# Kernel optimization log

Measured on AMD Instinct MI355X. Metric: run time of the kernel, lower is better.

Reference implementation:

```python
import jax, jax.numpy as jnp
import numpy as np
from jax import lax

B, C_IN, IMG, P = 8, 320, 64, 2
H = W = IMG // P            # 32
N = H * W                   # 1024 tokens
DIM = 128 * P * P           # 512
DEPTH, HEADS, DH = 6, 8, 64
INNER = HEADS * DH          # 512
MLP = 512
EPS = 1e-5


def layernorm(x, g, b):
    mu = x.mean(-1, keepdims=True)
    var = ((x - mu) ** 2).mean(-1, keepdims=True)
    return (x - mu) * lax.rsqrt(var + EPS) * g + b


def conv3x3(x, w, b):
    y = lax.conv_general_dilated(x, w, (1, 1), 'SAME',
                                 dimension_numbers=('NCHW', 'OIHW', 'NCHW'))
    return y + b[None, :, None, None]


def posemb_sincos_2d(h, w, dim, temperature=10000.0):
    y, x = jnp.meshgrid(jnp.arange(h, dtype=jnp.float32),
                        jnp.arange(w, dtype=jnp.float32), indexing='ij')
    omega = jnp.arange(dim // 4, dtype=jnp.float32) / (dim // 4 - 1)
    omega = 1.0 / (temperature ** omega)
    y = y.reshape(-1)[:, None] * omega[None, :]
    x = x.reshape(-1)[:, None] * omega[None, :]
    return jnp.concatenate([jnp.sin(x), jnp.cos(x), jnp.sin(y), jnp.cos(y)], axis=1)


def prepare_attn_mask(mask):
    # attn mask allows position pairs where either row or col token is marked.
    f = 64 // H
    m = (mask == 1)
    r = m.reshape(-1, H, f, W, f).any(axis=(2, 4)).reshape(-1, N)  # [M, N] bool
    return r[:, :, None] | r[:, None, :]                            # [M, N, N]


def setup_inputs() -> dict:
    key = jax.random.key(0)
    ks = jax.random.split(key, 24)
    s = 0.02
    d = dict(
        img=jax.random.normal(ks[0], (B, C_IN, IMG, IMG), jnp.float32),
        mask=jax.random.randint(ks[1], (DEPTH * B, 64, 64), 0, 2, jnp.int32),
        conv1_w=jax.random.normal(ks[2], (128, C_IN, 3, 3), jnp.float32) * s,
        conv1_b=jnp.zeros((128,), jnp.float32),
        ln_p_g=jnp.ones((DIM,), jnp.float32), ln_p_b=jnp.zeros((DIM,), jnp.float32),
        proj_w=jax.random.normal(ks[3], (DIM, DIM), jnp.float32) * s,
        proj_b=jnp.zeros((DIM,), jnp.float32),
        ln_q_g=jnp.ones((DIM,), jnp.float32), ln_q_b=jnp.zeros((DIM,), jnp.float32),
        attn_ln_g=jnp.ones((DEPTH, DIM), jnp.float32),
        attn_ln_b=jnp.zeros((DEPTH, DIM), jnp.float32),
        wqkv=jax.random.normal(ks[4], (DEPTH, DIM, 3 * INNER), jnp.float32) * s,
        wo=jax.random.normal(ks[5], (DEPTH, INNER, DIM), jnp.float32) * s,
        ff_ln_g=jnp.ones((DEPTH, DIM), jnp.float32),
        ff_ln_b=jnp.zeros((DEPTH, DIM), jnp.float32),
        w1=jax.random.normal(ks[6], (DEPTH, DIM, MLP), jnp.float32) * s,
        b1=jnp.zeros((DEPTH, MLP), jnp.float32),
        w2=jax.random.normal(ks[7], (DEPTH, MLP, DIM), jnp.float32) * s,
        b2=jnp.zeros((DEPTH, DIM), jnp.float32),
        conv2_w=jax.random.normal(ks[8], (C_IN, 128, 3, 3), jnp.float32) * s,
        conv2_b=jnp.zeros((C_IN,), jnp.float32),
    )
    return d


def reference(img, mask, conv1_w, conv1_b, ln_p_g, ln_p_b, proj_w, proj_b,
              ln_q_g, ln_q_b, attn_ln_g, attn_ln_b, wqkv, wo,
              ff_ln_g, ff_ln_b, w1, b1, w2, b2, conv2_w, conv2_b):
    am = prepare_attn_mask(mask).reshape(DEPTH, B, N, N)  # per-layer masks

    # patch embed: conv -> rearrange 'b c (h p1) (w p2) -> b (h w) (p1 p2 c)'
    y = conv3x3(img, conv1_w, conv1_b)                           # [B,128,64,64]
    y = y.reshape(B, 128, H, P, W, P).transpose(0, 2, 4, 3, 5, 1)
    y = y.reshape(B, N, P * P * 128)                             # [B,N,512]
    x = layernorm(y, ln_p_g, ln_p_b) @ proj_w + proj_b
    x = layernorm(x, ln_q_g, ln_q_b)
    x = x + posemb_sincos_2d(H, W, DIM).astype(x.dtype)

    scale = DH ** -0.5
    for i in range(DEPTH):
        xn = layernorm(x, attn_ln_g[i], attn_ln_b[i])
        qkv = xn @ wqkv[i]                                       # [B,N,3*INNER]
        q, k, v = jnp.split(qkv, 3, axis=-1)
        q, k, v = (t.reshape(B, N, HEADS, DH).transpose(0, 2, 1, 3)
                   for t in (q, k, v))
        dots = jnp.einsum('bhid,bhjd->bhij', q, k) * scale
        min_val = lax.stop_gradient(dots.min())
        dots = jnp.where(am[i][:, None, :, :], dots, min_val)
        attn = jax.nn.softmax(dots, axis=-1)
        o = jnp.einsum('bhij,bhjd->bhid', attn, v)
        o = o.transpose(0, 2, 1, 3).reshape(B, N, INNER) @ wo[i]
        x = o + x
        h = layernorm(x, ff_ln_g[i], ff_ln_b[i]) @ w1[i] + b1[i]
        x = jax.nn.gelu(h, approximate=False) @ w2[i] + b2[i] + x

    # 'b (h w) (p1 p2 c) -> b c (h p1) (w p2)' then conv
    z = x.reshape(B, H, W, P, P, 128).transpose(0, 5, 1, 3, 2, 4)
    z = z.reshape(B, 128, IMG, IMG)
    return conv3x3(z, conv2_w, conv2_b)
```

## Files before the change

kernel.cpp:

```cpp
#include <hip/hip_runtime.h>
#include <hip/hip_bf16.h>
#include <math.h>

typedef __attribute__((ext_vector_type(8))) short short8;
typedef __attribute__((ext_vector_type(4))) float f32x4;
typedef unsigned short u16;
typedef unsigned int u32;

#define DEV __device__ __forceinline__

DEV float bf2f(u16 u){ u32 x = ((u32)u)<<16; return __builtin_bit_cast(float, x); }
DEV u16 f2bf(float f){ u32 x = __builtin_bit_cast(u32, f); return (u16)((x + 0x7FFFu + ((x>>16)&1u))>>16); }
DEV f32x4 mfma16(short8 a, short8 b, f32x4 c){ return __builtin_amdgcn_mfma_f32_16x16x32_bf16(a,b,c,0,0,0); }
DEV void gload16(const void* g, void* l){
  __builtin_amdgcn_global_load_lds((const __attribute__((address_space(1))) void*)g,
                                   (__attribute__((address_space(3))) void*)l, 16, 0, 0);
}
DEV u32 fkey(float f){ u32 b = __builtin_bit_cast(u32, f); return (b & 0x80000000u) ? ~b : (b ^ 0x80000000u); }
DEV float funkey(u32 k){ u32 b = (k & 0x80000000u) ? (k ^ 0x80000000u) : ~k; return __builtin_bit_cast(float, b); }

static constexpr size_t O_PROJW = 0;
static constexpr size_t O_QKVW  = O_PROJW + 524288;
static constexpr size_t O_WOW   = O_QKVW + 9437184;
static constexpr size_t O_W1W   = O_WOW + 3145728;
static constexpr size_t O_W2W   = O_W1W + 3145728;
static constexpr size_t O_C1W   = O_W2W + 3145728;
static constexpr size_t O_C2W   = O_C1W + 737280;
static constexpr size_t O_RA    = O_C2W + 737280;
static constexpr size_t O_RB    = O_RA + 22302720;
static constexpr size_t O_X     = O_RB + 25165824;
static constexpr size_t O_D     = O_X + 16777216;
static constexpr size_t O_F     = O_D + 8388608;
static constexpr size_t O_RM    = O_F + 8388608;
static constexpr size_t O_MIN   = O_RM + 49152;
static constexpr size_t WS_NEED = O_MIN + 256;

__global__ __launch_bounds__(256) void k_transpose_bf(const float* __restrict__ src, u16* __restrict__ dst, int K, int N){
  __shared__ float tile[32][33];
  const int k0 = blockIdx.x*32, n0 = blockIdx.y*32;
  src += (size_t)blockIdx.z*K*N; dst += (size_t)blockIdx.z*K*N;
  const int c = threadIdx.x & 31, r4 = threadIdx.x >> 5;
  for(int r=r4; r<32; r+=8) tile[r][c] = src[(size_t)(k0+r)*N + n0+c];
  __syncthreads();
  for(int r=r4; r<32; r+=8) dst[(size_t)(n0+r)*K + k0+c] = f2bf(tile[c][r]);
}

__global__ __launch_bounds__(256) void k_convw(const float* __restrict__ src, u16* __restrict__ dst, int OC, int IC){
  int idx = blockIdx.x*256 + threadIdx.x;
  int total = OC*IC*9;
  if(idx >= total) return;
  int oc = idx/(IC*9); int rem = idx - oc*IC*9; int tap = rem/IC; int ic = rem - tap*IC;
  dst[idx] = f2bf(src[(size_t)(oc*IC+ic)*9 + tap]);
}

__global__ __launch_bounds__(256) void k_pad_img(const float* __restrict__ img, u16* __restrict__ pcl){
  const int by = blockIdx.x; const int b = by>>6, y = by&63; const int c0 = blockIdx.y*64;
  __shared__ float t[64][65];
  const int tx = threadIdx.x & 63, tz = threadIdx.x >> 6;
  for(int ci=tz; ci<64; ci+=4) t[ci][tx] = img[(((size_t)b*320 + c0+ci)*64 + y)*64 + tx];
  __syncthreads();
  for(int x=tz; x<64; x+=4) pcl[(((size_t)b*66 + y+1)*66 + (x+1))*320 + c0 + tx] = f2bf(t[tx][x]);
}

__global__ __launch_bounds__(256) void k_pad_tok(const float* __restrict__ x, u16* __restrict__ pcl){
  int idx = blockIdx.x*256 + threadIdx.x;
  const int c = idx & 127; int r = idx >> 7; const int xx = r & 63; r >>= 6; const int yy = r & 63; const int b = r >> 6;
  const int n = (yy>>1)*32 + (xx>>1); const int f = (yy&1)*256 + (xx&1)*128 + c;
  pcl[(((size_t)b*66 + yy+1)*66 + xx+1)*128 + c] = f2bf(x[((size_t)b*1024 + n)*512 + f]);
}

__global__ __launch_bounds__(256) void k_rmask(const int* __restrict__ mask, unsigned char* __restrict__ rm){
  int idx = blockIdx.x*256 + threadIdx.x;
  if(idx >= 48*1024) return;
  const int m = idx >> 10, n = idx & 1023; const int h = n>>5, w = n&31;
  const int* mp = mask + ((size_t)m*64 + h*2)*64 + w*2;
  rm[idx] = (unsigned char)((mp[0]==1) | (mp[1]==1) | (mp[64]==1) | (mp[65]==1));
}

__global__ __launch_bounds__(256) void k_vt(const u16* __restrict__ v, u16* __restrict__ vt){
  const int nt = blockIdx.x, bh = blockIdx.y;
  __shared__ u16 t[64][72];
  const int tid = threadIdx.x;
  const int i = tid>>2, cq = tid&3;
  const u16* src = v + ((size_t)bh*1024 + nt*64 + i)*64 + cq*16;
  const short8 s0 = *(const short8*)src;
  const short8 s1 = *(const short8*)(src+8);
  #pragma unroll
  for(int e=0;e<8;e++){ t[cq*16+e][i] = (u16)s0[e]; t[cq*16+8+e][i] = (u16)s1[e]; }
  __syncthreads();
  short8 o0, o1;
  #pragma unroll
  for(int e=0;e<8;e++){ o0[e] = (short)t[i][cq*16+e]; o1[e] = (short)t[i][cq*16+8+e]; }
  u16* dst = vt + (size_t)bh*65536 + (size_t)i*1024 + nt*64 + cq*16;
  *(short8*)dst = o0;
  *(short8*)(dst+8) = o1;
}

__global__ __launch_bounds__(256) void k_ln_bf(const float* __restrict__ in, const float* __restrict__ gw,
                                               const float* __restrict__ bw, u16* __restrict__ out){
  const int tok = blockIdx.x*4 + (threadIdx.x>>6);
  const int lane = threadIdx.x & 63;
  const float* rp = in + (size_t)tok*512 + lane*8;
  const float4 a = *(const float4*)rp;
  const float4 b = *(const float4*)(rp+4);
  float s  = a.x+a.y+a.z+a.w + b.x+b.y+b.z+b.w;
  float sq = a.x*a.x+a.y*a.y+a.z*a.z+a.w*a.w + b.x*b.x+b.y*b.y+b.z*b.z+b.w*b.w;
  #pragma unroll
  for(int off=1; off<64; off<<=1){ s += __shfl_xor(s,off); sq += __shfl_xor(sq,off); }
  const float mu = s*(1.f/512.f);
  const float rs = rsqrtf(sq*(1.f/512.f) - mu*mu + 1e-5f);
  const float4 g0 = *(const float4*)(gw + lane*8);
  const float4 g1 = *(const float4*)(gw + lane*8 + 4);
  const float4 b0 = *(const float4*)(bw + lane*8);
  const float4 b1 = *(const float4*)(bw + lane*8 + 4);
  short8 o8;
  o8[0]=f2bf((a.x-mu)*rs*g0.x+b0.x); o8[1]=f2bf((a.y-mu)*rs*g0.y+b0.y);
  o8[2]=f2bf((a.z-mu)*rs*g0.z+b0.z); o8[3]=f2bf((a.w-mu)*rs*g0.w+b0.w);
  o8[4]=f2bf((b.x-mu)*rs*g1.x+b1.x); o8[5]=f2bf((b.y-mu)*rs*g1.y+b1.y);
  o8[6]=f2bf((b.z-mu)*rs*g1.z+b1.z); o8[7]=f2bf((b.w-mu)*rs*g1.w+b1.w);
  *(short8*)(out + (size_t)tok*512 + lane*8) = o8;
}

__global__ __launch_bounds__(256) void k_lnq_pos(const float* __restrict__ in, const float* __restrict__ gw,
                                                 const float* __restrict__ bw, float* __restrict__ out){
  const int tok = blockIdx.x*4 + (threadIdx.x>>6);
  const int lane = threadIdx.x & 63;
  const float* rp = in + (size_t)tok*512 + lane*8;
  const float4 a = *(const float4*)rp;
  const float4 b = *(const float4*)(rp+4);
  float s  = a.x+a.y+a.z+a.w + b.x+b.y+b.z+b.w;
  float sq = a.x*a.x+a.y*a.y+a.z*a.z+a.w*a.w + b.x*b.x+b.y*b.y+b.z*b.z+b.w*b.w;
  #pragma unroll
  for(int off=1; off<64; off<<=1){ s += __shfl_xor(s,off); sq += __shfl_xor(sq,off); }
  const float mu = s*(1.f/512.f);
  const float rs = rsqrtf(sq*(1.f/512.f) - mu*mu + 1e-5f);
  const int n = tok & 1023; const int yy = n>>5, xx = n&31;
  const int f0 = lane*8; const int sec = f0>>7;
  const float coord = (sec<2) ? (float)xx : (float)yy;
  const float vv[8] = {a.x,a.y,a.z,a.w,b.x,b.y,b.z,b.w};
  float ov[8];
  #pragma unroll
  for(int j=0;j<8;j++){
    const int f = f0+j; const int qq = f & 127;
    const float om = __expf(-(float)qq * (9.2103403719761836f/127.f));
    const float arg = coord * om;
    const float pe = (sec&1) ? __cosf(arg) : __sinf(arg);
    ov[j] = (vv[j]-mu)*rs*gw[f] + bw[f] + pe;
  }
  float* op = out + (size_t)tok*512 + f0;
  *(float4*)op = (float4){ov[0],ov[1],ov[2],ov[3]};
  *(float4*)(op+4) = (float4){ov[4],ov[5],ov[6],ov[7]};
}

template<int EPI, int CONVC>
__global__ __launch_bounds__(256, 4)
void k_gemm(const u16* __restrict__ A, const u16* __restrict__ Wt,
            const float* __restrict__ bias, void* __restrict__ outp,
            const float* __restrict__ resid, int M, int N, int Kd)
{
  __shared__ u16 Ald[2][4096];
  __shared__ u16 Bld[2][4096];
  const int tid = threadIdx.x, lane = tid & 63, wv = tid >> 6;
  const int lr = lane & 15, g = lane >> 4;
  const int m0 = blockIdx.x * 64, n0 = blockIdx.y * 64;
  const int wm = (wv >> 1) * 32, wn = (wv & 1) * 32;
  const int srow = tid >> 3;
  const int sc  = (tid & 7) ^ (srow & 7);
  int b0=0, yy0=0, xx0=0;
  if constexpr (CONVC != 0){ b0 = m0>>12; yy0 = (m0>>6)&63; }
  const u16* arow0p; const u16* arow1p;
  if constexpr (CONVC != 0){
    arow0p = A; arow1p = A;
  } else {
    arow0p = A + (size_t)(m0+srow)*Kd + sc*8;
    arow1p = A + (size_t)(m0+srow+32)*Kd + sc*8;
  }
  const u16* brow0p = Wt + (size_t)(n0+srow)*Kd + sc*8;
  const u16* brow1p = Wt + (size_t)(n0+srow+32)*Kd + sc*8;

  f32x4 acc[2][2];
  #pragma unroll
  for(int i=0;i<2;i++)
    #pragma unroll
    for(int j=0;j<2;j++) acc[i][j] = (f32x4){0.f,0.f,0.f,0.f};

  const int nIter = Kd >> 6;
  int cur = 0;

  auto stage = [&](int kt, int buf){
    const int k0 = kt << 6;
    const u16 *ga0, *ga1;
    if constexpr (CONVC != 0){
      const int tap = k0 / CONVC;
      const int ic0 = k0 - tap*CONVC;
      const int ky = tap/3, kx = tap - 3*(tap/3);
      const size_t rb0 = ((size_t)((b0*66 + yy0+ky)*66 + kx))*CONVC + ic0 + sc*8;
      ga0 = A + rb0 + (size_t)(srow)*CONVC;
      ga1 = A + rb0 + (size_t)(srow+32)*CONVC;
    } else {
      ga0 = arow0p + k0;
      ga1 = arow1p + k0;
    }
    gload16(ga0, &Ald[buf][tid*8]);
    gload16(ga1, &Ald[buf][2048 + tid*8]);
    gload16(brow0p + k0, &Bld[buf][tid*8]);
    gload16(brow1p + k0, &Bld[buf][2048 + tid*8]);
  };

  stage(0, 0);
  for(int kt=0; kt<nIter; ++kt){
    __syncthreads();
    if(kt+1 < nIter) stage(kt+1, cur^1);
    short8 af[2][2], bg[2][2];
    #pragma unroll
    for(int mi=0;mi<2;mi++)
      #pragma unroll
      for(int kk=0;kk<2;kk++){
        const int R = wm + mi*16 + lr;
        const int Rn = wn + mi*16 + lr;
        const int c = kk*4 + g;
        af[mi][kk] = *(const short8*)&Ald[cur][R*64 + ((c ^ (R&7))<<3)];
        bg[mi][kk] = *(const short8*)&Bld[cur][Rn*64 + ((c ^ (Rn&7))<<3)];
      }
    #pragma unroll
    for(int mi=0;mi<2;mi++)
      #pragma unroll
      for(int nj=0;nj<2;nj++)
        #pragma unroll
        for(int kk=0;kk<2;kk++)
          acc[mi][nj] = mfma16(af[mi][kk], bg[nj][kk], acc[mi][nj]);
    cur ^= 1;
  }

  #pragma unroll
  for(int mi=0;mi<2;mi++){
    #pragma unroll
    for(int nj=0;nj<2;nj++){
      #pragma unroll
      for(int r=0;r<4;r++){
        const int mrow = m0 + wm + mi*16 + g*4 + r;
        const int ncol = n0 + wn + nj*16 + lr;
        float val = acc[mi][nj][r];
        if constexpr (EPI==0 || EPI==3 || EPI==4 || EPI==5 || EPI==6)
          val += bias[ncol];
        if constexpr (EPI==0){
          ((float*)outp)[(size_t)mrow*512 + ncol] = val;
        } else if constexpr (EPI==1){
          const int sec = ncol >> 9, rem = ncol & 511;
          const int head = rem >> 6, d = rem & 63;
          const int b = mrow >> 10, t = mrow & 1023;
          ((u16*)outp)[(size_t)sec*4194304 + ((size_t)((b*8+head)*1024 + t))*64 + d] = f2bf(val);
        } else if constexpr (EPI==2 || EPI==4){
          const size_t idx = (size_t)mrow*512 + ncol;
          ((float*)outp)[idx] = resid[idx] + val;
        } else if constexpr (EPI==3){
          const float gl = 0.5f * val * (1.f + erff(val * 0.70710678118654752f));
          ((u16*)outp)[(size_t)mrow*512 + ncol] = f2bf(gl);
        } else if constexpr (EPI==5){
          const int b = mrow>>12; const int rr = mrow&4095; const int y = rr>>6; const int xx = rr&63;
          const size_t pidx = ((size_t)(b*1024 + (y>>1)*32 + (xx>>1)))*512 + (y&1)*256 + (xx&1)*128 + ncol;
          ((float*)outp)[pidx] = val;
        } else if constexpr (EPI==6){
          const int b = mrow>>12; const int rr = mrow&4095; const int y = rr>>6; const int xx = rr&63;
          ((float*)outp)[(((size_t)(b*320 + ncol))*64 + y)*64 + xx] = val;
        }
      }
    }
  }
}

__global__ __launch_bounds__(256, 4)
void k_attn_min(const u16* __restrict__ q, const u16* __restrict__ k, u32* __restrict__ minbuf, int layer){
  const int qt = blockIdx.x, bh = blockIdx.y;
  __shared__ u16 Kld[2][4096];
  __shared__ float red[4];
  const int tid = threadIdx.x, lane = tid & 63, wv = tid >> 6;
  const int lr = lane & 15, g = lane >> 4;
  const u16* qp = q + ((size_t)bh*1024 + qt*64 + wv*16 + lr)*64;
  const short8 qa0 = *(const short8*)(qp + g*8);
  const short8 qa1 = *(const short8*)(qp + 32 + g*8);
  const u16* kbase = k + (size_t)bh*65536;
  const int srow = ((wv*64 + lane)>>3), scs = lane&7;
  const int scg = scs ^ (srow&7);
  const int srow2 = srow + 32;
  const int scg2 = scs ^ (srow2&7);
  float mn = 3.0e38f;
  gload16(kbase + (size_t)srow*64 + scg*8, &Kld[0][wv*512]);
  gload16(kbase + (size_t)srow2*64 + scg2*8, &Kld[0][2048 + wv*512]);
  int cur = 0;
  for(int jt=0; jt<16; ++jt){
    __syncthreads();
    if(jt < 15){
      const int j1 = (jt+1)*64;
      gload16(kbase + (size_t)(j1+srow)*64 + scg*8, &Kld[cur^1][wv*512]);
      gload16(kbase + (size_t)(j1+srow2)*64 + scg2*8, &Kld[cur^1][2048 + wv*512]);
    }
    #pragma unroll
    for(int c=0;c<4;c++){
      const int rr = c*16 + lr;
      const short8 kb0 = *(const short8*)&Kld[cur][rr*64 + ((g ^ (rr&7))<<3)];
      const short8 kb1 = *(const short8*)&Kld[cur][rr*64 + (((g+4) ^ (rr&7))<<3)];
      f32x4 s4 = (f32x4){0.f,0.f,0.f,0.f};
      s4 = mfma16(qa0, kb0, s4);
      s4 = mfma16(qa1, kb1, s4);
      mn = fminf(mn, fminf(fminf(s4[0],s4[1]), fminf(s4[2],s4[3])));
    }
    cur ^= 1;
  }
  mn *= 0.125f;
  #pragma unroll
  for(int off=32; off; off>>=1) mn = fminf(mn, __shfl_down(mn, off));
  if(lane==0) red[wv] = mn;
  __syncthreads();
  if(tid==0){
    const float m2 = fminf(fminf(red[0],red[1]), fminf(red[2],red[3]));
    atomicMin(minbuf + layer, fkey(m2));
  }
}

__global__ __launch_bounds__(256, 4)
void k_attn(const u16* __restrict__ q, const u16* __restrict__ k, const u16* __restrict__ vt,
            const unsigned char* __restrict__ rm, const u32* __restrict__ minbuf,
            u16* __restrict__ o, int layer){
  const int qt = blockIdx.x, bh = blockIdx.y; const int b = bh>>3, h = bh&7;
  __shared__ u16 Kld[2][4096];
  __shared__ u16 Vtld[2][4096];
  __shared__ u16 Pld[4][1024];
  const int tid = threadIdx.x, lane = tid & 63, wv = tid >> 6;
  const int lr = lane & 15, g = lane >> 4;
  const u16* qp = q + ((size_t)bh*1024 + qt*64 + wv*16 + lr)*64;
  const short8 qa0 = *(const short8*)(qp + g*8);
  const short8 qa1 = *(const short8*)(qp + 32 + g*8);
  const float SC = 0.125f * 1.44269504088896f;
  const float minv = funkey(minbuf[layer]) * 1.44269504088896f;
  const unsigned char* rmp = rm + (size_t)(layer*8 + b)*1024;
  bool rrow[4];
  #pragma unroll
  for(int r=0;r<4;r++) rrow[r] = rmp[qt*64 + wv*16 + g*4 + r] != 0;
  float mrun[4], lrun[4];
  #pragma unroll
  for(int r=0;r<4;r++){ mrun[r] = -3.0e38f; lrun[r] = 0.f; }
  f32x4 accd[4];
  #pragma unroll
  for(int d=0;d<4;d++) accd[d] = (f32x4){0.f,0.f,0.f,0.f};
  const u16* kbase = k + (size_t)bh*65536;
  const u16* vtbase = vt + (size_t)bh*65536;
  const int srow = ((wv*64 + lane)>>3), scs = lane&7;
  const int scg = scs ^ (srow&7);
  const int srow2 = srow + 32;
  const int scg2 = scs ^ (srow2&7);
  gload16(kbase + (size_t)srow*64 + scg*8, &Kld[0][wv*512]);
  gload16(kbase + (size_t)srow2*64 + scg2*8, &Kld[0][2048 + wv*512]);
  gload16(vtbase + (size_t)srow*1024 + scg*8, &Vtld[0][wv*512]);
  gload16(vtbase + (size_t)srow2*1024 + scg2*8, &Vtld[0][2048 + wv*512]);
  int cur = 0;
  for(int jt=0; jt<16; ++jt){
    const int j0 = jt*64;
    __syncthreads();
    if(jt < 15){
      const int j1 = j0 + 64;
      gload16(kbase + (size_t)(j1+srow)*64 + scg*8, &Kld[cur^1][wv*512]);
      gload16(kbase + (size_t)(j1+srow2)*64 + scg2*8, &Kld[cur^1][2048 + wv*512]);
      gload16(vtbase + (size_t)srow*1024 + j1 + scg*8, &Vtld[cur^1][wv*512]);
      gload16(vtbase + (size_t)srow2*1024 + j1 + scg2*8, &Vtld[cur^1][2048 + wv*512]);
    }
    float p4[4][4];
    #pragma unroll
    for(int c=0;c<4;c++){
      const int rr = c*16 + lr;
      const short8 kb0 = *(const short8*)&Kld[cur][rr*64 + ((g ^ (rr&7))<<3)];
      const short8 kb1 = *(const short8*)&Kld[cur][rr*64 + (((g+4) ^ (rr&7))<<3)];
      f32x4 s4 = (f32x4){0.f,0.f,0.f,0.f};
      s4 = mfma16(qa0, kb0, s4);
      s4 = mfma16(qa1, kb1, s4);
      const bool colok = rmp[j0 + rr] != 0;
      #pragma unroll
      for(int r=0;r<4;r++){
        float vl = s4[r]*SC;
        if(!(rrow[r] || colok)) vl = minv;
        p4[c][r] = vl;
      }
    }
    float sf[4];
    #pragma unroll
    for(int r=0;r<4;r++){
      float mx = fmaxf(fmaxf(p4[0][r],p4[1][r]), fmaxf(p4[2][r],p4[3][r]));
      mx = fmaxf(mx, __shfl_xor(mx,1)); mx = fmaxf(mx, __shfl_xor(mx,2));
      mx = fmaxf(mx, __shfl_xor(mx,4)); mx = fmaxf(mx, __shfl_xor(mx,8));
      const float mnew = fmaxf(mrun[r], mx);
      float ts = 0.f;
      #pragma unroll
      for(int c=0;c<4;c++){ const float e = exp2f(p4[c][r]-mnew); p4[c][r] = e; ts += e; }
      ts += __shfl_xor(ts,1); ts += __shfl_xor(ts,2); ts += __shfl_xor(ts,4); ts += __shfl_xor(ts,8);
      sf[r] = exp2f(mrun[r] - mnew);
      lrun[r] = lrun[r]*sf[r] + ts;
      mrun[r] = mnew;
    }
    #pragma unroll
    for(int d=0;d<4;d++)
      #pragma unroll
      for(int r=0;r<4;r++) accd[d][r] *= sf[r];
    #pragma unroll
    for(int c=0;c<4;c++)
      #pragma unroll
      for(int r=0;r<4;r++){
        const int ql = g*4+r, cl = c*16+lr;
        Pld[wv][ql*64 + ((((cl>>3) ^ (ql&7))<<3) | (cl&7))] = f2bf(p4[c][r]);
      }
    const short8 pa0 = *(const short8*)&Pld[wv][lr*64 + ((g ^ (lr&7))<<3)];
    const short8 pa1 = *(const short8*)&Pld[wv][lr*64 + (((g+4) ^ (lr&7))<<3)];
    #pragma unroll
    for(int d=0;d<4;d++){
      const int rr = d*16 + lr;
      const short8 vb0 = *(const short8*)&Vtld[cur][rr*64 + ((g ^ (rr&7))<<3)];
      const short8 vb1 = *(const short8*)&Vtld[cur][rr*64 + (((g+4) ^ (rr&7))<<3)];
      accd[d] = mfma16(pa0, vb0, accd[d]);
      accd[d] = mfma16(pa1, vb1, accd[d]);
    }
    cur ^= 1;
  }
  #pragma unroll
  for(int d=0;d<4;d++)
    #pragma unroll
    for(int r=0;r<4;r++){
      const int qrow = qt*64 + wv*16 + g*4 + r;
      o[((size_t)b*1024 + qrow)*512 + h*64 + d*16 + lr] = f2bf(accd[d][r] / lrun[r]);
    }
}

extern "C" void kernel_launch(void* const* d_in, const int* in_sizes, int n_in,
                              void* d_out, int out_size, void* d_ws, size_t ws_size,
                              hipStream_t stream)
{
  const float* img     = (const float*)d_in[0];
  const int*   mask    = (const int*)d_in[1];
  const float* conv1_w = (const float*)d_in[2];
  const float* conv1_b = (const float*)d_in[3];
  const float* ln_p_g  = (const float*)d_in[4];
  const float* ln_p_b  = (const float*)d_in[5];
  const float* proj_w  = (const float*)d_in[6];
  const float* proj_b  = (const float*)d_in[7];
  const float* ln_q_g  = (const float*)d_in[8];
  const float* ln_q_b  = (const float*)d_in[9];
  const float* attn_ln_g = (const float*)d_in[10];
  const float* attn_ln_b = (const float*)d_in[11];
  const float* wqkv    = (const float*)d_in[12];
  const float* wo      = (const float*)d_in[13];
  const float* ff_ln_g = (const float*)d_in[14];
  const float* ff_ln_b = (const float*)d_in[15];
  const float* w1      = (const float*)d_in[16];
  const float* b1      = (const float*)d_in[17];
  const float* w2      = (const float*)d_in[18];
  const float* b2      = (const float*)d_in[19];
  const float* conv2_w = (const float*)d_in[20];
  const float* conv2_b = (const float*)d_in[21];

  if(ws_size < WS_NEED) return;
  char* ws = (char*)d_ws;
  u16* projWt = (u16*)(ws + O_PROJW);
  u16* qkvWt  = (u16*)(ws + O_QKVW);
  u16* woWt   = (u16*)(ws + O_WOW);
  u16* w1Wt   = (u16*)(ws + O_W1W);
  u16* w2Wt   = (u16*)(ws + O_W2W);
  u16* c1Wt   = (u16*)(ws + O_C1W);
  u16* c2Wt   = (u16*)(ws + O_C2W);
  u16* pcl    = (u16*)(ws + O_RA);
  float* tmpf = (float*)(ws + O_RA);
  u16* vtb    = (u16*)(ws + O_RA);
  float* patches = (float*)(ws + O_RB);
  u16* qkvb   = (u16*)(ws + O_RB);
  float* xbuf = (float*)(ws + O_X);
  u16* xnbf   = (u16*)(ws + O_D);
  u16* obf    = (u16*)(ws + O_F);
  unsigned char* rmb = (unsigned char*)(ws + O_RM);
  u32* minbuf = (u32*)(ws + O_MIN);

  hipMemsetAsync(ws + O_MIN, 0xFF, 64, stream);
  hipMemsetAsync(ws + O_RA, 0, 22302720, stream);

  k_transpose_bf<<<dim3(16,16,1),256,0,stream>>>(proj_w, projWt, 512, 512);
  k_transpose_bf<<<dim3(16,48,6),256,0,stream>>>(wqkv,   qkvWt,  512, 1536);
  k_transpose_bf<<<dim3(16,16,6),256,0,stream>>>(wo,     woWt,   512, 512);
  k_transpose_bf<<<dim3(16,16,6),256,0,stream>>>(w1,     w1Wt,   512, 512);
  k_transpose_bf<<<dim3(16,16,6),256,0,stream>>>(w2,     w2Wt,   512, 512);
  k_convw<<<1440,256,0,stream>>>(conv1_w, c1Wt, 128, 320);
  k_convw<<<1440,256,0,stream>>>(conv2_w, c2Wt, 320, 128);
  k_rmask<<<192,256,0,stream>>>(mask, rmb);

  k_pad_img<<<dim3(512,5),256,0,stream>>>(img, pcl);
  k_gemm<5,320><<<dim3(512,2),256,0,stream>>>(pcl, c1Wt, conv1_b, patches, nullptr, 32768, 128, 2880);
  k_ln_bf<<<2048,256,0,stream>>>(patches, ln_p_g, ln_p_b, xnbf);
  k_gemm<0,0><<<dim3(128,8),256,0,stream>>>(xnbf, projWt, proj_b, tmpf, nullptr, 8192, 512, 512);
  k_lnq_pos<<<2048,256,0,stream>>>(tmpf, ln_q_g, ln_q_b, xbuf);

  const u16* qb = qkvb;
  const u16* kb = qkvb + 4194304;
  const u16* vb = qkvb + 8388608;
  for(int i=0;i<6;i++){
    k_ln_bf<<<2048,256,0,stream>>>(xbuf, attn_ln_g + i*512, attn_ln_b + i*512, xnbf);
    k_gemm<1,0><<<dim3(128,24),256,0,stream>>>(xnbf, qkvWt + (size_t)i*1536*512, nullptr, qkvb, nullptr, 8192, 1536, 512);
    k_vt<<<dim3(16,64),256,0,stream>>>(vb, vtb);
    k_attn_min<<<dim3(16,64),256,0,stream>>>(qb, kb, minbuf, i);
    k_attn<<<dim3(16,64),256,0,stream>>>(qb, kb, vtb, rmb, minbuf, obf, i);
    k_gemm<2,0><<<dim3(128,8),256,0,stream>>>(obf, woWt + (size_t)i*512*512, nullptr, xbuf, xbuf, 8192, 512, 512);
    k_ln_bf<<<2048,256,0,stream>>>(xbuf, ff_ln_g + i*512, ff_ln_b + i*512, xnbf);
    k_gemm<3,0><<<dim3(128,8),256,0,stream>>>(xnbf, w1Wt + (size_t)i*512*512, b1 + i*512, obf, nullptr, 8192, 512, 512);
    k_gemm<4,0><<<dim3(128,8),256,0,stream>>>(obf, w2Wt + (size_t)i*512*512, b2 + i*512, xbuf, xbuf, 8192, 512, 512);
  }

  hipMemsetAsync(ws + O_RA, 0, 8921088, stream);
  k_pad_tok<<<16384,256,0,stream>>>(xbuf, pcl);
  k_gemm<6,128><<<dim3(512,5),256,0,stream>>>(pcl, c2Wt, conv2_b, d_out, nullptr, 32768, 320, 1152);
}
```

Baseline: 1.128 ms.

## Use global max bound for softmax, drop online rescaling and LDS staging

The min pre-pass now also computes a global max of the scaled scores per layer. The attention kernel subtracts that fixed max instead of keeping a running per-row max, which removes the per-tile max reduction, the rescale of accumulators and the row-sum shuffles inside the loop. K and V^T are now read straight from global memory into registers instead of double-buffered LDS via async loads. Block ids are remapped so the 8 heads of a batch are spread across neighbouring blocks. The risk is underflow of exp for rows whose max sits far below the global max, plus more global and L2 traffic without LDS reuse.

```diff
diff --git a/kernel.cpp b/kernel.cpp
--- a/kernel.cpp
+++ b/kernel.cpp
@@ -166,7 +166,7 @@
   const int wm = (wv >> 1) * 32, wn = (wv & 1) * 32;
   const int srow = tid >> 3;
   const int sc  = (tid & 7) ^ (srow & 7);
-  int b0=0, yy0=0, xx0=0;
+  int b0=0, yy0=0;
   if constexpr (CONVC != 0){ b0 = m0>>12; yy0 = (m0>>6)&63; }
   const u16* arow0p; const u16* arow1p;
   if constexpr (CONVC != 0){
@@ -270,136 +270,104 @@
 }
 
 __global__ __launch_bounds__(256, 4)
-void k_attn_min(const u16* __restrict__ q, const u16* __restrict__ k, u32* __restrict__ minbuf, int layer){
-  const int qt = blockIdx.x, bh = blockIdx.y;
-  __shared__ u16 Kld[2][4096];
-  __shared__ float red[4];
+void k_attn_minmax(const u16* __restrict__ q, const u16* __restrict__ k, u32* __restrict__ keys, int layer){
+  const int id = blockIdx.x;
+  const int qt = (id>>3)&15;
+  const int bh = ((id&7)<<3) | (id>>7);
   const int tid = threadIdx.x, lane = tid & 63, wv = tid >> 6;
   const int lr = lane & 15, g = lane >> 4;
   const u16* qp = q + ((size_t)bh*1024 + qt*64 + wv*16 + lr)*64;
   const short8 qa0 = *(const short8*)(qp + g*8);
   const short8 qa1 = *(const short8*)(qp + 32 + g*8);
   const u16* kbase = k + (size_t)bh*65536;
-  const int srow = ((wv*64 + lane)>>3), scs = lane&7;
-  const int scg = scs ^ (srow&7);
-  const int srow2 = srow + 32;
-  const int scg2 = scs ^ (srow2&7);
-  float mn = 3.0e38f;
-  gload16(kbase + (size_t)srow*64 + scg*8, &Kld[0][wv*512]);
-  gload16(kbase + (size_t)srow2*64 + scg2*8, &Kld[0][2048 + wv*512]);
-  int cur = 0;
+  float mn = 3.0e38f, mx = -3.0e38f;
   for(int jt=0; jt<16; ++jt){
-    __syncthreads();
-    if(jt < 15){
-      const int j1 = (jt+1)*64;
-      gload16(kbase + (size_t)(j1+srow)*64 + scg*8, &Kld[cur^1][wv*512]);
-      gload16(kbase + (size_t)(j1+srow2)*64 + scg2*8, &Kld[cur^1][2048 + wv*512]);
-    }
+    const int j0 = jt*64;
     #pragma unroll
     for(int c=0;c<4;c++){
-      const int rr = c*16 + lr;
-      const short8 kb0 = *(const short8*)&Kld[cur][rr*64 + ((g ^ (rr&7))<<3)];
-      const short8 kb1 = *(const short8*)&Kld[cur][rr*64 + (((g+4) ^ (rr&7))<<3)];
+      const u16* kp = kbase + (size_t)(j0 + c*16 + lr)*64 + g*8;
+      const short8 kb0 = *(const short8*)kp;
+      const short8 kb1 = *(const short8*)(kp + 32);
       f32x4 s4 = (f32x4){0.f,0.f,0.f,0.f};
       s4 = mfma16(qa0, kb0, s4);
       s4 = mfma16(qa1, kb1, s4);
       mn = fminf(mn, fminf(fminf(s4[0],s4[1]), fminf(s4[2],s4[3])));
-    }
-    cur ^= 1;
-  }
-  mn *= 0.125f;
-  #pragma unroll
-  for(int off=32; off; off>>=1) mn = fminf(mn, __shfl_down(mn, off));
-  if(lane==0) red[wv] = mn;
-  __syncthreads();
-  if(tid==0){
-    const float m2 = fminf(fminf(red[0],red[1]), fminf(red[2],red[3]));
-    atomicMin(minbuf + layer, fkey(m2));
+      mx = fmaxf(mx, fmaxf(fmaxf(s4[0],s4[1]), fmaxf(s4[2],s4[3])));
+    }
+  }
+  mn *= 0.125f; mx *= 0.125f;
+  #pragma unroll
+  for(int off=32; off; off>>=1){
+    mn = fminf(mn, __shfl_down(mn, off));
+    mx = fmaxf(mx, __shfl_down(mx, off));
+  }
+  if(lane==0){
+    atomicMin(keys + layer, fkey(mn));
+    atomicMax(keys + 8 + layer, fkey(mx));
   }
 }
 
 __global__ __launch_bounds__(256, 4)
 void k_attn(const u16* __restrict__ q, const u16* __restrict__ k, const u16* __restrict__ vt,
-            const unsigned char* __restrict__ rm, const u32* __restrict__ minbuf,
+            const unsigned char* __restrict__ rm, const u32* __restrict__ keys,
             u16* __restrict__ o, int layer){
-  const int qt = blockIdx.x, bh = blockIdx.y; const int b = bh>>3, h = bh&7;
-  __shared__ u16 Kld[2][4096];
-  __shared__ u16 Vtld[2][4096];
+  const int id = blockIdx.x;
+  const int qt = (id>>3)&15;
+  const int bh = ((id&7)<<3) | (id>>7);
+  const int b = bh>>3, h = bh&7;
   __shared__ u16 Pld[4][1024];
   const int tid = threadIdx.x, lane = tid & 63, wv = tid >> 6;
   const int lr = lane & 15, g = lane >> 4;
   const u16* qp = q + ((size_t)bh*1024 + qt*64 + wv*16 + lr)*64;
   const short8 qa0 = *(const short8*)(qp + g*8);
   const short8 qa1 = *(const short8*)(qp + 32 + g*8);
-  const float SC = 0.125f * 1.44269504088896f;
-  const float minv = funkey(minbuf[layer]) * 1.44269504088896f;
+  const float L2E = 1.44269504088896f;
+  const float SC = 0.125f * L2E;
+  const float minvE = funkey(keys[layer]) * L2E;
+  const float ME    = funkey(keys[8+layer]) * L2E;
   const unsigned char* rmp = rm + (size_t)(layer*8 + b)*1024;
   bool rrow[4];
   #pragma unroll
   for(int r=0;r<4;r++) rrow[r] = rmp[qt*64 + wv*16 + g*4 + r] != 0;
-  float mrun[4], lrun[4];
-  #pragma unroll
-  for(int r=0;r<4;r++){ mrun[r] = -3.0e38f; lrun[r] = 0.f; }
+  float lrun[4] = {0.f,0.f,0.f,0.f};
   f32x4 accd[4];
   #pragma unroll
   for(int d=0;d<4;d++) accd[d] = (f32x4){0.f,0.f,0.f,0.f};
   const u16* kbase = k + (size_t)bh*65536;
   const u16* vtbase = vt + (size_t)bh*65536;
-  const int srow = ((wv*64 + lane)>>3), scs = lane&7;
-  const int scg = scs ^ (srow&7);
-  const int srow2 = srow + 32;
-  const int scg2 = scs ^ (srow2&7);
-  gload16(kbase + (size_t)srow*64 + scg*8, &Kld[0][wv*512]);
-  gload16(kbase + (size_t)srow2*64 + scg2*8, &Kld[0][2048 + wv*512]);
-  gload16(vtbase + (size_t)srow*1024 + scg*8, &Vtld[0][wv*512]);
-  gload16(vtbase + (size_t)srow2*1024 + scg2*8, &Vtld[0][2048 + wv*512]);
-  int cur = 0;
+
   for(int jt=0; jt<16; ++jt){
     const int j0 = jt*64;
-    __syncthreads();
-    if(jt < 15){
-      const int j1 = j0 + 64;
-      gload16(kbase + (size_t)(j1+srow)*64 + scg*8, &Kld[cur^1][wv*512]);
-      gload16(kbase + (size_t)(j1+srow2)*64 + scg2*8, &Kld[cur^1][2048 + wv*512]);
-      gload16(vtbase + (size_t)srow*1024 + j1 + scg*8, &Vtld[cur^1][wv*512]);
-      gload16(vtbase + (size_t)srow2*1024 + j1 + scg2*8, &Vtld[cur^1][2048 + wv*512]);
-    }
-    float p4[4][4];
+    f32x4 s4c[4];
     #pragma unroll
     for(int c=0;c<4;c++){
-      const int rr = c*16 + lr;
-      const short8 kb0 = *(const short8*)&Kld[cur][rr*64 + ((g ^ (rr&7))<<3)];
-      const short8 kb1 = *(const short8*)&Kld[cur][rr*64 + (((g+4) ^ (rr&7))<<3)];
+      const u16* kp = kbase + (size_t)(j0 + c*16 + lr)*64 + g*8;
+      const short8 kb0 = *(const short8*)kp;
+      const short8 kb1 = *(const short8*)(kp + 32);
       f32x4 s4 = (f32x4){0.f,0.f,0.f,0.f};
       s4 = mfma16(qa0, kb0, s4);
-      s4 = mfma16(qa1, kb1, s4);
-      const bool colok = rmp[j0 + rr] != 0;
+      s4c[c] = mfma16(qa1, kb1, s4);
+    }
+    short8 vb[4][2];
+    #pragma unroll
+    for(int d=0;d<4;d++){
+      const u16* vp = vtbase + (size_t)(d*16 + lr)*1024 + j0 + g*8;
+      vb[d][0] = *(const short8*)vp;
+      vb[d][1] = *(const short8*)(vp + 32);
+    }
+    float p4[4][4];
+    #pragma unroll
+    for(int c=0;c<4;c++){
+      const bool colok = rmp[j0 + c*16 + lr] != 0;
       #pragma unroll
       for(int r=0;r<4;r++){
-        float vl = s4[r]*SC;
-        if(!(rrow[r] || colok)) vl = minv;
-        p4[c][r] = vl;
+        const float vl = (rrow[r] | colok) ? s4c[c][r]*SC : minvE;
+        p4[c][r] = exp2f(vl - ME);
       }
     }
-    float sf[4];
-    #pragma unroll
-    for(int r=0;r<4;r++){
-      float mx = fmaxf(fmaxf(p4[0][r],p4[1][r]), fmaxf(p4[2][r],p4[3][r]));
-      mx = fmaxf(mx, __shfl_xor(mx,1)); mx = fmaxf(mx, __shfl_xor(mx,2));
-      mx = fmaxf(mx, __shfl_xor(mx,4)); mx = fmaxf(mx, __shfl_xor(mx,8));
-      const float mnew = fmaxf(mrun[r], mx);
-      float ts = 0.f;
-      #pragma unroll
-      for(int c=0;c<4;c++){ const float e = exp2f(p4[c][r]-mnew); p4[c][r] = e; ts += e; }
-      ts += __shfl_xor(ts,1); ts += __shfl_xor(ts,2); ts += __shfl_xor(ts,4); ts += __shfl_xor(ts,8);
-      sf[r] = exp2f(mrun[r] - mnew);
-      lrun[r] = lrun[r]*sf[r] + ts;
-      mrun[r] = mnew;
-    }
-    #pragma unroll
-    for(int d=0;d<4;d++)
-      #pragma unroll
-      for(int r=0;r<4;r++) accd[d][r] *= sf[r];
+    #pragma unroll
+    for(int r=0;r<4;r++)
+      lrun[r] += (p4[0][r]+p4[1][r]) + (p4[2][r]+p4[3][r]);
     #pragma unroll
     for(int c=0;c<4;c++)
       #pragma unroll
@@ -411,20 +379,24 @@
     const short8 pa1 = *(const short8*)&Pld[wv][lr*64 + (((g+4) ^ (lr&7))<<3)];
     #pragma unroll
     for(int d=0;d<4;d++){
-      const int rr = d*16 + lr;
-      const short8 vb0 = *(const short8*)&Vtld[cur][rr*64 + ((g ^ (rr&7))<<3)];
-      const short8 vb1 = *(const short8*)&Vtld[cur][rr*64 + (((g+4) ^ (rr&7))<<3)];
-      accd[d] = mfma16(pa0, vb0, accd[d]);
-      accd[d] = mfma16(pa1, vb1, accd[d]);
-    }
-    cur ^= 1;
+      accd[d] = mfma16(pa0, vb[d][0], accd[d]);
+      accd[d] = mfma16(pa1, vb[d][1], accd[d]);
+    }
+  }
+  float inv[4];
+  #pragma unroll
+  for(int r=0;r<4;r++){
+    float ls = lrun[r];
+    ls += __shfl_xor(ls,1); ls += __shfl_xor(ls,2);
+    ls += __shfl_xor(ls,4); ls += __shfl_xor(ls,8);
+    inv[r] = 1.f / ls;
   }
   #pragma unroll
   for(int d=0;d<4;d++)
     #pragma unroll
     for(int r=0;r<4;r++){
       const int qrow = qt*64 + wv*16 + g*4 + r;
-      o[((size_t)b*1024 + qrow)*512 + h*64 + d*16 + lr] = f2bf(accd[d][r] / lrun[r]);
+      o[((size_t)b*1024 + qrow)*512 + h*64 + d*16 + lr] = f2bf(accd[d][r] * inv[r]);
     }
 }
 
@@ -475,7 +447,8 @@
   unsigned char* rmb = (unsigned char*)(ws + O_RM);
   u32* minbuf = (u32*)(ws + O_MIN);
 
-  hipMemsetAsync(ws + O_MIN, 0xFF, 64, stream);
+  hipMemsetAsync(ws + O_MIN, 0xFF, 32, stream);
+  hipMemsetAsync(ws + O_MIN + 32, 0, 32, stream);
   hipMemsetAsync(ws + O_RA, 0, 22302720, stream);
 
   k_transpose_bf<<<dim3(16,16,1),256,0,stream>>>(proj_w, projWt, 512, 512);
@@ -500,8 +473,8 @@
     k_ln_bf<<<2048,256,0,stream>>>(xbuf, attn_ln_g + i*512, attn_ln_b + i*512, xnbf);
     k_gemm<1,0><<<dim3(128,24),256,0,stream>>>(xnbf, qkvWt + (size_t)i*1536*512, nullptr, qkvb, nullptr, 8192, 1536, 512);
     k_vt<<<dim3(16,64),256,0,stream>>>(vb, vtb);
-    k_attn_min<<<dim3(16,64),256,0,stream>>>(qb, kb, minbuf, i);
-    k_attn<<<dim3(16,64),256,0,stream>>>(qb, kb, vtb, rmb, minbuf, obf, i);
+    k_attn_minmax<<<1024,256,0,stream>>>(qb, kb, minbuf, i);
+    k_attn<<<1024,256,0,stream>>>(qb, kb, vtb, rmb, minbuf, obf, i);
     k_gemm<2,0><<<dim3(128,8),256,0,stream>>>(obf, woWt + (size_t)i*512*512, nullptr, xbuf, xbuf, 8192, 512, 512);
     k_ln_bf<<<2048,256,0,stream>>>(xbuf, ff_ln_g + i*512, ff_ln_b + i*512, xnbf);
     k_gemm<3,0><<<dim3(128,8),256,0,stream>>>(xnbf, w1Wt + (size_t)i*512*512, b1 + i*512, obf, nullptr, 8192, 512, 512);
```

After: 2.094 ms. 85.6% more time.
